# Optimization experiments

Measured on AMD Instinct MI355X. Metric: run time of the kernel, lower is better.

Reference implementation:

```python
import jax, jax.numpy as jnp
import numpy as np

B, T, D, H = 4, 1024, 1024, 16
DH = D // H  # 64

def setup_inputs() -> dict:
    key = jax.random.key(0)
    ks = jax.random.split(key, 5)
    s = 1.0 / np.sqrt(D)
    return {
        "x": jax.random.normal(ks[0], (B, T, D), dtype=jnp.float32),
        "Wqkv": jax.random.uniform(ks[1], (D, 3 * D), dtype=jnp.float32, minval=-s, maxval=s),
        "bqkv": jax.random.uniform(ks[2], (3 * D,), dtype=jnp.float32, minval=-s, maxval=s),
        "Wproj": jax.random.uniform(ks[3], (D, D), dtype=jnp.float32, minval=-s, maxval=s),
        "bproj": jax.random.uniform(ks[4], (D,), dtype=jnp.float32, minval=-s, maxval=s),
        "mask": jnp.ones((B, T), dtype=jnp.int32),
    }

def reference(x, Wqkv, bqkv, Wproj, bproj, mask):
    Bx, Tx, C = x.shape
    qkv = x @ Wqkv + bqkv                      # [B,T,3D]
    q, k, v = jnp.split(qkv, 3, axis=-1)
    # [B,H,T,DH]
    q = q.reshape(Bx, Tx, H, DH).transpose(0, 2, 1, 3)
    k = k.reshape(Bx, Tx, H, DH).transpose(0, 2, 1, 3)
    v = v.reshape(Bx, Tx, H, DH).transpose(0, 2, 1, 3)
    att = jnp.einsum("bhqd,bhkd->bhqk", q, k) / np.sqrt(DH)
    causal = jnp.tril(jnp.ones((Tx, Tx), dtype=bool))          # [T,T]
    keep = causal[None, None] & (mask[:, None, None, :] != 0)  # [B,1,T,T] broadcast
    att = jnp.where(keep, att, -jnp.inf)
    att = jax.nn.softmax(att, axis=-1)
    # dropout is identity in eval / p=0
    out = jnp.einsum("bhqk,bhkd->bhqd", att, v)                # [B,H,T,DH]
    out = out.transpose(0, 2, 1, 3).reshape(Bx, Tx, C)
    return out @ Wproj + bproj
```

## Files before the change

kernel.cpp:

```cpp
#include <hip/hip_runtime.h>
#include <hip/hip_bf16.h>
#include <cstddef>
#include <cstdint>

#define Bb 4
#define Tt 1024
#define Dd 1024
#define Hh 16

typedef __bf16 bf16x8 __attribute__((ext_vector_type(8)));
typedef __bf16 bf16x4 __attribute__((ext_vector_type(4)));
typedef float  f32x4  __attribute__((ext_vector_type(4)));

__device__ __forceinline__ void gload16(const void* g, void* l) {
    __builtin_amdgcn_global_load_lds(
        (const __attribute__((address_space(1))) void*)g,
        (__attribute__((address_space(3))) void*)l, 16, 0, 0);
}

#define VMC6() asm volatile("s_waitcnt vmcnt(6)" ::: "memory")
#define VMC4() asm volatile("s_waitcnt vmcnt(4)" ::: "memory")
#define VMC0() asm volatile("s_waitcnt vmcnt(0)" ::: "memory")
#define RAWBAR() asm volatile("s_barrier" ::: "memory")

__global__ __launch_bounds__(256) void prep(const float* __restrict__ x,
                                            const float* __restrict__ Wqkv,
                                            const float* __restrict__ Wproj,
                                            __bf16* __restrict__ xb,
                                            __bf16* __restrict__ wqT,
                                            __bf16* __restrict__ wpT) {
    const int bid = blockIdx.x;
    if (bid < 4096) {
        int i = bid * 256 + threadIdx.x;
        float4 v = ((const float4*)x)[i];
        bf16x4 o = { (__bf16)v.x, (__bf16)v.y, (__bf16)v.z, (__bf16)v.w };
        ((bf16x4*)xb)[i] = o;
        return;
    }
    __shared__ float ld[64][65];
    const float* in;
    __bf16* out;
    int K, N, k0, n0;
    if (bid < 4096 + 768) {
        int j = bid - 4096;
        in = Wqkv; out = wqT; K = 1024; N = 3072;
        k0 = (j & 15) * 64; n0 = (j >> 4) * 64;
    } else {
        int j = bid - 4096 - 768;
        in = Wproj; out = wpT; K = 1024; N = 1024;
        k0 = (j & 15) * 64; n0 = (j >> 4) * 64;
    }
    #pragma unroll
    for (int i = 0; i < 16; i++) {
        int idx = i * 256 + threadIdx.x;
        int r = idx >> 6, c = idx & 63;
        ld[r][c] = in[(size_t)(k0 + r) * N + n0 + c];
    }
    __syncthreads();
    #pragma unroll
    for (int i = 0; i < 4; i++) {
        int idx = i * 256 + threadIdx.x;
        int r = idx >> 4, c4 = (idx & 15) * 4;
        bf16x4 o = { (__bf16)ld[c4][r], (__bf16)ld[c4 + 1][r],
                     (__bf16)ld[c4 + 2][r], (__bf16)ld[c4 + 3][r] };
        *(bf16x4*)&out[(size_t)(n0 + r) * K + k0 + c4] = o;
    }
}

__global__ __launch_bounds__(256) void gemm_qkv(const __bf16* __restrict__ A,
                                                const __bf16* __restrict__ Bt,
                                                const float* __restrict__ bias,
                                                __bf16* __restrict__ Cout,
                                                __bf16* __restrict__ vt,
                                                int M, int N, int K) {
    __shared__ __align__(16) __bf16 smem[24576];

    const int tid  = threadIdx.x;
    const int lane = tid & 63;
    const int wave = tid >> 6;
    const int wy = wave >> 1, wx = wave & 1;
    const int l15 = lane & 15, quad = lane >> 4;
    const size_t row0 = (size_t)blockIdx.y * 128;
    const size_t col0 = (size_t)blockIdx.x * 128;

    f32x4 acc[4][4] = {};

    const int c0 = tid, c1 = 256 + tid;
    const int r0 = c0 >> 2, s0 = (c0 & 3) ^ ((r0 >> 1) & 3);
    const int r1 = c1 >> 2, s1 = (c1 & 3) ^ ((r1 >> 1) & 3);

#define STAGE(it, buf) do {                                                   \
        const int _k0 = (it) << 5;                                            \
        gload16(&A[(row0 + r0) * K + _k0 + s0 * 8], &(buf)[c0 * 8]);          \
        gload16(&Bt[(col0 + r0) * K + _k0 + s0 * 8], &(buf)[4096 + c0 * 8]);  \
        gload16(&A[(row0 + r1) * K + _k0 + s1 * 8], &(buf)[c1 * 8]);          \
        gload16(&Bt[(col0 + r1) * K + _k0 + s1 * 8], &(buf)[4096 + c1 * 8]);  \
    } while (0)

    __bf16 *b0 = smem, *b1 = smem + 8192, *b2 = smem + 16384;
    STAGE(0, b0);
    STAGE(1, b1);

    const int niter = K >> 5;
    for (int it = 0; it < niter; it++) {
        if (it + 1 < niter) VMC4(); else VMC0();
        RAWBAR();
        if (it + 2 < niter) STAGE(it + 2, b2);

        bf16x8 af[4], bfr[4];
        #pragma unroll
        for (int i = 0; i < 4; i++) {
            const int r = wy * 64 + i * 16 + l15;
            af[i] = *(const bf16x8*)&b0[r * 32 + ((quad ^ ((r >> 1) & 3)) * 8)];
        }
        #pragma unroll
        for (int j = 0; j < 4; j++) {
            const int r = wx * 64 + j * 16 + l15;
            bfr[j] = *(const bf16x8*)&b0[4096 + r * 32 + ((quad ^ ((r >> 1) & 3)) * 8)];
        }
        #pragma unroll
        for (int i = 0; i < 4; i++)
            #pragma unroll
            for (int j = 0; j < 4; j++)
                acc[i][j] = __builtin_amdgcn_mfma_f32_16x16x32_bf16(af[i], bfr[j], acc[i][j], 0, 0, 0);

        __bf16* tswap = b0; b0 = b1; b1 = b2; b2 = tswap;
    }
#undef STAGE

    __syncthreads();
    const float scale = (col0 < 1024) ? 0.125f : 1.0f;
    #pragma unroll
    for (int j = 0; j < 4; j++) {
        const int cl = wx * 64 + j * 16 + l15;
        const float bj = bias[col0 + cl];
        #pragma unroll
        for (int i = 0; i < 4; i++) {
            const int rl = wy * 64 + i * 16 + quad * 4;
            #pragma unroll
            for (int r = 0; r < 4; r++)
                smem[(rl + r) * 132 + cl] = (__bf16)((acc[i][j][r] + bj) * scale);
        }
    }
    __syncthreads();
    if (col0 < 2048) {
        #pragma unroll
        for (int p = 0; p < 8; p++) {
            const int row = p * 16 + (tid >> 4);
            const int ch  = tid & 15;
            bf16x8 v = *(const bf16x8*)&smem[row * 132 + ch * 8];
            *(bf16x8*)&Cout[(row0 + row) * N + col0 + ch * 8] = v;
        }
    } else {
        const int bidx = (int)(row0 >> 10);
        const int t0g  = (int)(row0 & 1023);
        const int cl   = tid >> 1;
        const int half = tid & 1;
        const int hd   = (int)(col0 - 2048) + cl;
        const size_t vrow = ((size_t)((bidx * Hh + (hd >> 6)) * 64 + (hd & 63))) * Tt + t0g;
        #pragma unroll
        for (int s = 0; s < 8; s++) {
            const int t = half * 64 + s * 8;
            bf16x8 v;
            #pragma unroll
            for (int u = 0; u < 8; u++) v[u] = smem[(t + u) * 132 + cl];
            *(bf16x8*)&vt[vrow + t] = v;
        }
    }
}

__device__ __forceinline__ void stage_proj(const __bf16* __restrict__ A,
                                           const __bf16* __restrict__ Bt,
                                           size_t row0, size_t col0, int K, int k0,
                                           __bf16* buf, int tid) {
    #pragma unroll
    for (int i = 0; i < 4; i++) {
        int c = i * 256 + tid;
        int r = c >> 3, seg = (c & 7) ^ (r & 7);
        gload16(&A[(row0 + r) * K + k0 + seg * 8], &buf[c * 8]);
    }
    #pragma unroll
    for (int i = 0; i < 2; i++) {
        int c = i * 256 + tid;
        int r = c >> 3, seg = (c & 7) ^ (r & 7);
        gload16(&Bt[(col0 + r) * K + k0 + seg * 8], &buf[8192 + c * 8]);
    }
}

__global__ __launch_bounds__(256) void gemm_bf16_n64(const __bf16* __restrict__ A,
                                                     const __bf16* __restrict__ Bt,
                                                     const float* __restrict__ bias,
                                                     float* __restrict__ Cout,
                                                     int M, int N, int K) {
    __shared__ __align__(16) __bf16 smem[36864];
    const int tid  = threadIdx.x;
    const int lane = tid & 63;
    const int wave = tid >> 6;
    const int wy = wave >> 1, wx = wave & 1;
    const int l15 = lane & 15, quad = lane >> 4;
    const size_t row0 = (size_t)blockIdx.y * 128;
    const size_t col0 = (size_t)blockIdx.x * 64;

    f32x4 acc[4][2] = {};

    __bf16 *b0 = smem, *b1 = smem + 12288, *b2 = smem + 24576;
    stage_proj(A, Bt, row0, col0, K, 0, b0, tid);
    stage_proj(A, Bt, row0, col0, K, 64, b1, tid);

    const int niter = K >> 6;
    for (int it = 0; it < niter; ++it) {
        if (it + 1 < niter) VMC6(); else VMC0();
        RAWBAR();
        if (it + 2 < niter) stage_proj(A, Bt, row0, col0, K, (it + 2) << 6, b2, tid);

        #pragma unroll
        for (int kc = 0; kc < 2; kc++) {
            bf16x8 af[4], bfr[2];
            #pragma unroll
            for (int i = 0; i < 4; i++)
                af[i] = *(const bf16x8*)&b0[(wy * 64 + i * 16 + l15) * 64 +
                                            (((kc * 4 + quad) ^ (l15 & 7)) * 8)];
            #pragma unroll
            for (int j = 0; j < 2; j++)
                bfr[j] = *(const bf16x8*)&b0[8192 + (wx * 32 + j * 16 + l15) * 64 +
                                             (((kc * 4 + quad) ^ (l15 & 7)) * 8)];
            #pragma unroll
            for (int i = 0; i < 4; i++)
                #pragma unroll
                for (int j = 0; j < 2; j++)
                    acc[i][j] = __builtin_amdgcn_mfma_f32_16x16x32_bf16(af[i], bfr[j], acc[i][j], 0, 0, 0);
        }

        __bf16* tswap = b0; b0 = b1; b1 = b2; b2 = tswap;
    }

    #pragma unroll
    for (int j = 0; j < 2; j++) {
        const size_t col = col0 + wx * 32 + j * 16 + l15;
        const float bj = bias[col];
        #pragma unroll
        for (int i = 0; i < 4; i++) {
            const size_t row = row0 + wy * 64 + i * 16 + quad * 4;
            #pragma unroll
            for (int r = 0; r < 4; r++)
                Cout[(row + r) * N + col] = acc[i][j][r] + bj;
        }
    }
}

__global__ __launch_bounds__(256, 4) void attn_mfma(const __bf16* __restrict__ qkv,
                                                    const __bf16* __restrict__ vt,
                                                    const int* __restrict__ mask,
                                                    __bf16* __restrict__ att) {
    __shared__ __align__(16) __bf16 Ks[2][4096];
    __shared__ __align__(16) __bf16 Vs[2][4096];
    __shared__ __align__(16) __bf16 Ps[4][1024];

    const int h  = blockIdx.x & 15;
    const int b  = blockIdx.x >> 4;
    const int qt = 15 - blockIdx.y;
    const int tid = threadIdx.x, lane = tid & 63, wave = tid >> 6;
    const int l15 = lane & 15, quad = lane >> 4;

    #pragma unroll
    for (int i = 0; i < 2; i++) {
        int c = i * 256 + tid;
        int rr = c >> 3, ch = c & 7;
        gload16(&qkv[((size_t)(b * Tt + qt * 64 + rr)) * 3072 + h * 64 + ((ch ^ (rr & 7)) * 8)],
                &Ks[0][c * 8]);
    }

    uint32_t mlo = 0, mhi = 0;
    for (int p = 0; p < 16; p++) {
        unsigned long long bal = __ballot(mask[b * Tt + p * 64 + lane] != 0);
        if ((lane & 15) == p) { mlo = (uint32_t)bal; mhi = (uint32_t)(bal >> 32); }
    }

    __syncthreads();
    bf16x8 qf0 = *(const bf16x8*)&Ks[0][(wave * 16 + l15) * 64 + ((quad ^ (l15 & 7)) * 8)];
    bf16x8 qf1 = *(const bf16x8*)&Ks[0][(wave * 16 + l15) * 64 + (((4 + quad) ^ (l15 & 7)) * 8)];
    __syncthreads();

    #pragma unroll
    for (int i = 0; i < 2; i++) {
        int c = i * 256 + tid;
        int rr = c >> 3, ch = c & 7, sw = ((ch ^ (rr & 7)) * 8);
        gload16(&qkv[((size_t)(b * Tt + rr)) * 3072 + 1024 + h * 64 + sw], &Ks[0][c * 8]);
        gload16(&vt[((size_t)((b * Hh + h) * 64 + rr)) * Tt + sw], &Vs[0][c * 8]);
    }

    f32x4 Oacc[4] = {};
    float lsum = 0.0f;

    for (int kt = 0; kt <= qt; kt++) {
        __syncthreads();
        const int cur = kt & 1;
        if (kt < qt) {
            #pragma unroll
            for (int i = 0; i < 2; i++) {
                int c = i * 256 + tid;
                int rr = c >> 3, ch = c & 7, sw = ((ch ^ (rr & 7)) * 8);
                gload16(&qkv[((size_t)(b * Tt + (kt + 1) * 64 + rr)) * 3072 + 1024 + h * 64 + sw],
                        &Ks[cur ^ 1][c * 8]);
                gload16(&vt[((size_t)((b * Hh + h) * 64 + rr)) * Tt + (kt + 1) * 64 + sw],
                        &Vs[cur ^ 1][c * 8]);
            }
        }

        const uint32_t lo = (uint32_t)__builtin_amdgcn_readlane((int)mlo, kt);
        const uint32_t hi = (uint32_t)__builtin_amdgcn_readlane((int)mhi, kt);

        bf16x8 ak[4][2];
        #pragma unroll
        for (int j = 0; j < 4; j++)
            #pragma unroll
            for (int kc = 0; kc < 2; kc++)
                ak[j][kc] = *(const bf16x8*)&Ks[cur][(j * 16 + l15) * 64 +
                                                     (((kc * 4 + quad) ^ (l15 & 7)) * 8)];
        #pragma unroll
        for (int j = 0; j < 4; j++) {
            f32x4 st = {};
            st = __builtin_amdgcn_mfma_f32_16x16x32_bf16(ak[j][0], qf0, st, 0, 0, 0);
            st = __builtin_amdgcn_mfma_f32_16x16x32_bf16(ak[j][1], qf1, st, 0, 0, 0);
            const uint32_t fld = (j < 2) ? (lo >> (j * 16)) : (hi >> ((j - 2) * 16));
            bf16x4 pv;
            #pragma unroll
            for (int r = 0; r < 4; r++) {
                const int tloc = j * 16 + quad * 4 + r;
                bool keep = (fld >> (quad * 4 + r)) & 1;
                if (kt == qt) keep = keep && (tloc <= wave * 16 + l15);
                const float pe = keep ? __expf(st[r]) : 0.0f;
                lsum += pe;
                pv[r] = (__bf16)pe;
            }
            *(bf16x4*)&Ps[wave][l15 * 64 + (((j * 4 + quad) ^ ((l15 & 7) << 1)) * 4)] = pv;
        }

        bf16x8 av[4][2];
        #pragma unroll
        for (int n = 0; n < 4; n++)
            #pragma unroll
            for (int kc = 0; kc < 2; kc++)
                av[n][kc] = *(const bf16x8*)&Vs[cur][(n * 16 + l15) * 64 +
                                                     (((kc * 4 + quad) ^ (l15 & 7)) * 8)];
        bf16x8 p0 = *(const bf16x8*)&Ps[wave][l15 * 64 + (((2 * quad) ^ ((l15 & 7) << 1)) * 4)];
        bf16x8 p1 = *(const bf16x8*)&Ps[wave][l15 * 64 + (((2 * (4 + quad)) ^ ((l15 & 7) << 1)) * 4)];
        #pragma unroll
        for (int n = 0; n < 4; n++) {
            Oacc[n] = __builtin_amdgcn_mfma_f32_16x16x32_bf16(av[n][0], p0, Oacc[n], 0, 0, 0);
            Oacc[n] = __builtin_amdgcn_mfma_f32_16x16x32_bf16(av[n][1], p1, Oacc[n], 0, 0, 0);
        }
    }

    float lt = lsum;
    lt += __shfl_xor(lt, 16);
    lt += __shfl_xor(lt, 32);
    const float inv = 1.0f / lt;
    const int q = qt * 64 + wave * 16 + l15;
    #pragma unroll
    for (int n = 0; n < 4; n++) {
        bf16x4 o;
        #pragma unroll
        for (int r = 0; r < 4; r++) o[r] = (__bf16)(Oacc[n][r] * inv);
        *(bf16x4*)&att[((size_t)(b * Tt + q)) * Dd + h * 64 + n * 16 + quad * 4] = o;
    }
}

extern "C" void kernel_launch(void* const* d_in, const int* in_sizes, int n_in,
                              void* d_out, int out_size, void* d_ws, size_t ws_size,
                              hipStream_t stream) {
    const float* x     = (const float*)d_in[0];
    const float* Wqkv  = (const float*)d_in[1];
    const float* bqkv  = (const float*)d_in[2];
    const float* Wproj = (const float*)d_in[3];
    const float* bproj = (const float*)d_in[4];
    const int*   mask  = (const int*)d_in[5];
    float* out = (float*)d_out;

    __bf16* xb  = (__bf16*)d_ws;
    __bf16* wqT = xb  + (size_t)4096 * 1024;
    __bf16* wpT = wqT + (size_t)3072 * 1024;
    __bf16* qkv = wpT + (size_t)1024 * 1024;
    __bf16* vt  = qkv + (size_t)4096 * 3072;
    __bf16* att = vt  + (size_t)4 * 16 * 64 * 1024;

    prep<<<4096 + 768 + 256, 256, 0, stream>>>(x, Wqkv, Wproj, xb, wqT, wpT);

    gemm_qkv<<<dim3(24, 32), 256, 0, stream>>>(xb, wqT, bqkv, qkv, vt, 4096, 3072, 1024);

    attn_mfma<<<dim3(64, 16), 256, 0, stream>>>(qkv, vt, mask, att);

    gemm_bf16_n64<<<dim3(16, 32), 256, 0, stream>>>(att, wpT, bproj, out, 4096, 1024, 1024);
}
```

Baseline: 157.5 us.

## Double-buffer GEMM fragments in registers to overlap LDS reads with MFMA

The GEMM main loop is unrolled by two and uses two register fragment sets. Fragments for the next K-tile are read from LDS while MFMAs run on the current tile, hiding LDS read latency behind matrix math. In exchange, every half-iteration now waits on all outstanding global loads (vmcnt 0) instead of leaving one stage in flight. That shortens the effective global prefetch distance, and the extra fragment registers raise register pressure.

```diff
diff --git a/kernel.cpp b/kernel.cpp
--- a/kernel.cpp
+++ b/kernel.cpp
@@ -97,36 +97,51 @@
         gload16(&Bt[(col0 + r1) * K + _k0 + s1 * 8], &(buf)[4096 + c1 * 8]);  \
     } while (0)
 
+#define LDFRAGS(buf, AF, BF) do {                                             \
+        _Pragma("unroll")                                                     \
+        for (int i = 0; i < 4; i++) {                                         \
+            const int r = wy * 64 + i * 16 + l15;                             \
+            AF[i] = *(const bf16x8*)&(buf)[r * 32 + ((quad ^ ((r >> 1) & 3)) * 8)]; \
+        }                                                                     \
+        _Pragma("unroll")                                                     \
+        for (int j = 0; j < 4; j++) {                                         \
+            const int r = wx * 64 + j * 16 + l15;                             \
+            BF[j] = *(const bf16x8*)&(buf)[4096 + r * 32 + ((quad ^ ((r >> 1) & 3)) * 8)]; \
+        }                                                                     \
+    } while (0)
+
+#define MFMA_ALL(AF, BF) do {                                                 \
+        _Pragma("unroll")                                                     \
+        for (int i = 0; i < 4; i++)                                           \
+            _Pragma("unroll")                                                 \
+            for (int j = 0; j < 4; j++)                                       \
+                acc[i][j] = __builtin_amdgcn_mfma_f32_16x16x32_bf16(          \
+                    AF[i], BF[j], acc[i][j], 0, 0, 0);                        \
+    } while (0)
+
     __bf16 *b0 = smem, *b1 = smem + 8192, *b2 = smem + 16384;
     STAGE(0, b0);
     STAGE(1, b1);
+    VMC4(); RAWBAR();
+    bf16x8 afA[4], bfA[4], afB[4], bfB[4];
+    LDFRAGS(b0, afA, bfA);
 
     const int niter = K >> 5;
-    for (int it = 0; it < niter; it++) {
-        if (it + 1 < niter) VMC4(); else VMC0();
-        RAWBAR();
+    for (int it = 0; it < niter; it += 2) {
+        VMC0(); RAWBAR();
         if (it + 2 < niter) STAGE(it + 2, b2);
-
-        bf16x8 af[4], bfr[4];
-        #pragma unroll
-        for (int i = 0; i < 4; i++) {
-            const int r = wy * 64 + i * 16 + l15;
-            af[i] = *(const bf16x8*)&b0[r * 32 + ((quad ^ ((r >> 1) & 3)) * 8)];
-        }
-        #pragma unroll
-        for (int j = 0; j < 4; j++) {
-            const int r = wx * 64 + j * 16 + l15;
-            bfr[j] = *(const bf16x8*)&b0[4096 + r * 32 + ((quad ^ ((r >> 1) & 3)) * 8)];
-        }
-        #pragma unroll
-        for (int i = 0; i < 4; i++)
-            #pragma unroll
-            for (int j = 0; j < 4; j++)
-                acc[i][j] = __builtin_amdgcn_mfma_f32_16x16x32_bf16(af[i], bfr[j], acc[i][j], 0, 0, 0);
-
-        __bf16* tswap = b0; b0 = b1; b1 = b2; b2 = tswap;
+        LDFRAGS(b1, afB, bfB);
+        MFMA_ALL(afA, bfA);
+        { __bf16* t = b0; b0 = b1; b1 = b2; b2 = t; }
+        VMC0(); RAWBAR();
+        if (it + 3 < niter) STAGE(it + 3, b2);
+        if (it + 2 < niter) LDFRAGS(b1, afA, bfA);
+        MFMA_ALL(afB, bfB);
+        { __bf16* t = b0; b0 = b1; b1 = b2; b2 = t; }
     }
 #undef STAGE
+#undef LDFRAGS
+#undef MFMA_ALL
 
     __syncthreads();
     const float scale = (col0 < 1024) ? 0.125f : 1.0f;
```

Measured after the change: 161.5 us. 1.03x slower.

## Double attention query tile to 128 rows so each K/V tile serves two Q blocks

Applied to the files above, without the earlier changes.

Each attention block now handles 128 query rows instead of 64. Each wave computes two 16-row query sub-tiles against every loaded K/V tile, so K/V global loads and LDS reads are reused across twice as many queries. The grid halves to 8 query tiles and the causal diagonal handling is generalized to a limit per key tile. In exchange, each thread holds more registers (launch bounds drop to 2 blocks/SM), there are fewer blocks in flight, and the causal load imbalance between blocks grows.

```diff
diff --git a/kernel.cpp b/kernel.cpp
--- a/kernel.cpp
+++ b/kernel.cpp
@@ -248,25 +248,25 @@
     }
 }
 
-__global__ __launch_bounds__(256, 4) void attn_mfma(const __bf16* __restrict__ qkv,
+__global__ __launch_bounds__(256, 2) void attn_mfma(const __bf16* __restrict__ qkv,
                                                     const __bf16* __restrict__ vt,
                                                     const int* __restrict__ mask,
                                                     __bf16* __restrict__ att) {
     __shared__ __align__(16) __bf16 Ks[2][4096];
     __shared__ __align__(16) __bf16 Vs[2][4096];
-    __shared__ __align__(16) __bf16 Ps[4][1024];
+    __shared__ __align__(16) __bf16 Ps[4][2048];
 
     const int h  = blockIdx.x & 15;
     const int b  = blockIdx.x >> 4;
-    const int qt = 15 - blockIdx.y;
+    const int qt = 7 - blockIdx.y;
     const int tid = threadIdx.x, lane = tid & 63, wave = tid >> 6;
     const int l15 = lane & 15, quad = lane >> 4;
 
     #pragma unroll
-    for (int i = 0; i < 2; i++) {
+    for (int i = 0; i < 4; i++) {
         int c = i * 256 + tid;
         int rr = c >> 3, ch = c & 7;
-        gload16(&qkv[((size_t)(b * Tt + qt * 64 + rr)) * 3072 + h * 64 + ((ch ^ (rr & 7)) * 8)],
+        gload16(&qkv[((size_t)(b * Tt + qt * 128 + rr)) * 3072 + h * 64 + ((ch ^ (rr & 7)) * 8)],
                 &Ks[0][c * 8]);
     }
 
@@ -277,8 +277,12 @@
     }
 
     __syncthreads();
-    bf16x8 qf0 = *(const bf16x8*)&Ks[0][(wave * 16 + l15) * 64 + ((quad ^ (l15 & 7)) * 8)];
-    bf16x8 qf1 = *(const bf16x8*)&Ks[0][(wave * 16 + l15) * 64 + (((4 + quad) ^ (l15 & 7)) * 8)];
+    const __bf16* const Kall = &Ks[0][0];
+    const int x7 = l15 & 7;
+    bf16x8 qfA0 = *(const bf16x8*)&Kall[(wave * 32 + l15) * 64 + ((quad ^ x7) * 8)];
+    bf16x8 qfA1 = *(const bf16x8*)&Kall[(wave * 32 + l15) * 64 + (((4 + quad) ^ x7) * 8)];
+    bf16x8 qfB0 = *(const bf16x8*)&Kall[(wave * 32 + 16 + l15) * 64 + ((quad ^ x7) * 8)];
+    bf16x8 qfB1 = *(const bf16x8*)&Kall[(wave * 32 + 16 + l15) * 64 + (((4 + quad) ^ x7) * 8)];
     __syncthreads();
 
     #pragma unroll
@@ -289,13 +293,14 @@
         gload16(&vt[((size_t)((b * Hh + h) * 64 + rr)) * Tt + sw], &Vs[0][c * 8]);
     }
 
-    f32x4 Oacc[4] = {};
-    float lsum = 0.0f;
-
-    for (int kt = 0; kt <= qt; kt++) {
+    f32x4 OA[4] = {}, OB[4] = {};
+    float lsA = 0.0f, lsB = 0.0f;
+    const int ktmax = 2 * qt + 1;
+
+    for (int kt = 0; kt <= ktmax; kt++) {
         __syncthreads();
         const int cur = kt & 1;
-        if (kt < qt) {
+        if (kt < ktmax) {
             #pragma unroll
             for (int i = 0; i < 2; i++) {
                 int c = i * 256 + tid;
@@ -309,6 +314,8 @@
 
         const uint32_t lo = (uint32_t)__builtin_amdgcn_readlane((int)mlo, kt);
         const uint32_t hi = (uint32_t)__builtin_amdgcn_readlane((int)mhi, kt);
+        const bool diag = (kt >= 2 * qt);
+        const int dlim = (2 * qt - kt) * 64;
 
         bf16x8 ak[4][2];
         #pragma unroll
@@ -316,24 +323,44 @@
             #pragma unroll
             for (int kc = 0; kc < 2; kc++)
                 ak[j][kc] = *(const bf16x8*)&Ks[cur][(j * 16 + l15) * 64 +
-                                                     (((kc * 4 + quad) ^ (l15 & 7)) * 8)];
+                                                     (((kc * 4 + quad) ^ x7) * 8)];
         #pragma unroll
         for (int j = 0; j < 4; j++) {
             f32x4 st = {};
-            st = __builtin_amdgcn_mfma_f32_16x16x32_bf16(ak[j][0], qf0, st, 0, 0, 0);
-            st = __builtin_amdgcn_mfma_f32_16x16x32_bf16(ak[j][1], qf1, st, 0, 0, 0);
+            st = __builtin_amdgcn_mfma_f32_16x16x32_bf16(ak[j][0], qfA0, st, 0, 0, 0);
+            st = __builtin_amdgcn_mfma_f32_16x16x32_bf16(ak[j][1], qfA1, st, 0, 0, 0);
             const uint32_t fld = (j < 2) ? (lo >> (j * 16)) : (hi >> ((j - 2) * 16));
+            const int lim = wave * 32 + l15 + dlim;
             bf16x4 pv;
             #pragma unroll
             for (int r = 0; r < 4; r++) {
                 const int tloc = j * 16 + quad * 4 + r;
                 bool keep = (fld >> (quad * 4 + r)) & 1;
-                if (kt == qt) keep = keep && (tloc <= wave * 16 + l15);
+                if (diag) keep = keep && (tloc <= lim);
                 const float pe = keep ? __expf(st[r]) : 0.0f;
-                lsum += pe;
+                lsA += pe;
                 pv[r] = (__bf16)pe;
             }
-            *(bf16x4*)&Ps[wave][l15 * 64 + (((j * 4 + quad) ^ ((l15 & 7) << 1)) * 4)] = pv;
+            *(bf16x4*)&Ps[wave][l15 * 64 + (((j * 4 + quad) ^ (x7 << 1)) * 4)] = pv;
+        }
+        #pragma unroll
+        for (int j = 0; j < 4; j++) {
+            f32x4 st = {};
+            st = __builtin_amdgcn_mfma_f32_16x16x32_bf16(ak[j][0], qfB0, st, 0, 0, 0);
+            st = __builtin_amdgcn_mfma_f32_16x16x32_bf16(ak[j][1], qfB1, st, 0, 0, 0);
+            const uint32_t fld = (j < 2) ? (lo >> (j * 16)) : (hi >> ((j - 2) * 16));
+            const int lim = wave * 32 + 16 + l15 + dlim;
+            bf16x4 pv;
+            #pragma unroll
+            for (int r = 0; r < 4; r++) {
+                const int tloc = j * 16 + quad * 4 + r;
+                bool keep = (fld >> (quad * 4 + r)) & 1;
+                if (diag) keep = keep && (tloc <= lim);
+                const float pe = keep ? __expf(st[r]) : 0.0f;
+                lsB += pe;
+                pv[r] = (__bf16)pe;
+            }
+            *(bf16x4*)&Ps[wave][(16 + l15) * 64 + (((j * 4 + quad) ^ (x7 << 1)) * 4)] = pv;
         }
 
         bf16x8 av[4][2];
@@ -342,27 +369,36 @@
             #pragma unroll
             for (int kc = 0; kc < 2; kc++)
                 av[n][kc] = *(const bf16x8*)&Vs[cur][(n * 16 + l15) * 64 +
-                                                     (((kc * 4 + quad) ^ (l15 & 7)) * 8)];
-        bf16x8 p0 = *(const bf16x8*)&Ps[wave][l15 * 64 + (((2 * quad) ^ ((l15 & 7) << 1)) * 4)];
-        bf16x8 p1 = *(const bf16x8*)&Ps[wave][l15 * 64 + (((2 * (4 + quad)) ^ ((l15 & 7) << 1)) * 4)];
+                                                     (((kc * 4 + quad) ^ x7) * 8)];
+        bf16x8 pA0 = *(const bf16x8*)&Ps[wave][l15 * 64 + (((2 * quad) ^ (x7 << 1)) * 4)];
+        bf16x8 pA1 = *(const bf16x8*)&Ps[wave][l15 * 64 + (((2 * (4 + quad)) ^ (x7 << 1)) * 4)];
+        bf16x8 pB0 = *(const bf16x8*)&Ps[wave][(16 + l15) * 64 + (((2 * quad) ^ (x7 << 1)) * 4)];
+        bf16x8 pB1 = *(const bf16x8*)&Ps[wave][(16 + l15) * 64 + (((2 * (4 + quad)) ^ (x7 << 1)) * 4)];
         #pragma unroll
         for (int n = 0; n < 4; n++) {
-            Oacc[n] = __builtin_amdgcn_mfma_f32_16x16x32_bf16(av[n][0], p0, Oacc[n], 0, 0, 0);
-            Oacc[n] = __builtin_amdgcn_mfma_f32_16x16x32_bf16(av[n][1], p1, Oacc[n], 0, 0, 0);
-        }
-    }
-
-    float lt = lsum;
-    lt += __shfl_xor(lt, 16);
-    lt += __shfl_xor(lt, 32);
-    const float inv = 1.0f / lt;
-    const int q = qt * 64 + wave * 16 + l15;
+            OA[n] = __builtin_amdgcn_mfma_f32_16x16x32_bf16(av[n][0], pA0, OA[n], 0, 0, 0);
+            OA[n] = __builtin_amdgcn_mfma_f32_16x16x32_bf16(av[n][1], pA1, OA[n], 0, 0, 0);
+            OB[n] = __builtin_amdgcn_mfma_f32_16x16x32_bf16(av[n][0], pB0, OB[n], 0, 0, 0);
+            OB[n] = __builtin_amdgcn_mfma_f32_16x16x32_bf16(av[n][1], pB1, OB[n], 0, 0, 0);
+        }
+    }
+
+    float ltA = lsA;
+    ltA += __shfl_xor(ltA, 16);
+    ltA += __shfl_xor(ltA, 32);
+    float ltB = lsB;
+    ltB += __shfl_xor(ltB, 16);
+    ltB += __shfl_xor(ltB, 32);
+    const float invA = 1.0f / ltA;
+    const float invB = 1.0f / ltB;
+    const int qA = qt * 128 + wave * 32 + l15;
     #pragma unroll
     for (int n = 0; n < 4; n++) {
-        bf16x4 o;
-        #pragma unroll
-        for (int r = 0; r < 4; r++) o[r] = (__bf16)(Oacc[n][r] * inv);
-        *(bf16x4*)&att[((size_t)(b * Tt + q)) * Dd + h * 64 + n * 16 + quad * 4] = o;
+        bf16x4 oa, ob;
+        #pragma unroll
+        for (int r = 0; r < 4; r++) { oa[r] = (__bf16)(OA[n][r] * invA); ob[r] = (__bf16)(OB[n][r] * invB); }
+        *(bf16x4*)&att[((size_t)(b * Tt + qA)) * Dd + h * 64 + n * 16 + quad * 4] = oa;
+        *(bf16x4*)&att[((size_t)(b * Tt + qA + 16)) * Dd + h * 64 + n * 16 + quad * 4] = ob;
     }
 }
 
@@ -388,7 +424,7 @@
 
     gemm_qkv<<<dim3(24, 32), 256, 0, stream>>>(xb, wqT, bqkv, qkv, vt, 4096, 3072, 1024);
 
-    attn_mfma<<<dim3(64, 16), 256, 0, stream>>>(qkv, vt, mask, att);
+    attn_mfma<<<dim3(64, 8), 256, 0, stream>>>(qkv, vt, mask, att);
 
     gemm_bf16_n64<<<dim3(16, 32), 256, 0, stream>>>(att, wpT, bproj, out, 4096, 1024, 1024);
 }
```

Result: slower. 169.5 us (+7.7%).
